# Kernel optimization log

Hardware: AMD Instinct MI355X
Metric: run time of the kernel (lower is better)

The kernel has to match this reference:

```python
import jax, jax.numpy as jnp
import numpy as np

B, S, D = 2, 2048, 1024
H, DH = 16, 64  # num_head, head_dim; H*DH == D


def setup_inputs() -> dict:
    key = jax.random.key(0)
    ks = jax.random.split(key, 10)
    stdv = 1.0 / np.sqrt(D)
    def lin(k):
        kw, kb = jax.random.split(k)
        W = jax.random.uniform(kw, (D, D), jnp.float32, -stdv, stdv)
        b = jax.random.uniform(kb, (D,), jnp.float32, -stdv, stdv)
        return W, b
    Wq, bq = lin(ks[0]); Wk, bk = lin(ks[1]); Wv, bv = lin(ks[2]); Wo, bo = lin(ks[3])
    x = jax.random.normal(ks[4], (B, S, D), jnp.float32)
    # causal mask: True = attend
    mask = jnp.tril(jnp.ones((S, S), jnp.bool_))
    mask = jnp.broadcast_to(mask, (B, S, S))
    return {"x": x, "mask": mask, "Wq": Wq, "bq": bq, "Wk": Wk, "bk": bk,
            "Wv": Wv, "bv": bv, "Wo": Wo, "bo": bo}


def _split_head(t):
    # [B,S,D] -> [B*H, S, DH]
    return t.reshape(B, S, H, DH).transpose(0, 2, 1, 3).reshape(B * H, S, DH)


def _concat_head(t):
    # [B*H, S, DH] -> [B, S, D]
    return t.reshape(B, H, S, DH).transpose(0, 2, 1, 3).reshape(B, S, D)


def reference(x, mask, Wq, bq, Wk, bk, Wv, bv, Wo, bo):
    q = _split_head(x @ Wq.T + bq)
    k = _split_head(x @ Wk.T + bk)
    v = _split_head(x @ Wv.T + bv)
    scale = 1.0 / jnp.sqrt(jnp.float32(DH))
    # scores: [B, H, S, S], masked softmax (flash-attention math, unfused ref)
    scores = jnp.einsum('nqd,nkd->nqk', q, k).reshape(B, H, S, S) * scale
    scores = jnp.where(mask[:, None, :, :], scores, jnp.finfo(scores.dtype).min)
    attn = jax.nn.softmax(scores, axis=-1)
    out = jnp.einsum('bhqk,nkd->bhqd', attn, v.reshape(B, H, S, DH).reshape(B * H, S, DH)).reshape(B * H, S, DH) if False else jnp.einsum('nqk,nkd->nqd', attn.reshape(B * H, S, S), v)
    return _concat_head(out) @ Wo.T + bo
```

## Files before the change

kernel.cpp:

```cpp
#include <hip/hip_runtime.h>
#include <cstdint>

#define S_LEN  2048
#define NH     16
#define DHEAD  64
#define DMODEL 1024

typedef __bf16 bf16x8 __attribute__((ext_vector_type(8)));
typedef __bf16 bf16x2 __attribute__((ext_vector_type(2)));
typedef float  f32x4  __attribute__((ext_vector_type(4)));

__device__ __forceinline__ unsigned short f2bf(float x) {
  union { float f; unsigned int u; } c; c.f = x;
  unsigned int u = c.u;
  return (unsigned short)((u + 0x7fffu + ((u >> 16) & 1u)) >> 16);
}

__device__ __forceinline__ unsigned int pkbf(float a, float b) {
#if __has_builtin(__builtin_amdgcn_cvt_pk_bf16_f32)
  bf16x2 r = __builtin_amdgcn_cvt_pk_bf16_f32(a, b);
  return *(unsigned int*)&r;
#else
  return (unsigned int)f2bf(a) | ((unsigned int)f2bf(b) << 16);
#endif
}

__device__ __forceinline__ unsigned short f2bf1(float x) {
#if __has_builtin(__builtin_amdgcn_cvt_pk_bf16_f32)
  bf16x2 r = __builtin_amdgcn_cvt_pk_bf16_f32(x, x);
  union { bf16x2 v; unsigned int u; } c; c.v = r;
  return (unsigned short)(c.u & 0xffffu);
#else
  return f2bf(x);
#endif
}

__device__ __forceinline__ __bf16 us2bf(unsigned short u) {
  union { unsigned short u; __bf16 b; } c; c.u = u; return c.b;
}

__device__ __forceinline__ void glds16(const void* g, void* l) {
  __builtin_amdgcn_global_load_lds(
      (const __attribute__((address_space(1))) void*)g,
      (__attribute__((address_space(3))) void*)l, 16, 0, 0);
}

__device__ __forceinline__ f32x4 mfma16(bf16x8 a, bf16x8 b, f32x4 c) {
  return __builtin_amdgcn_mfma_f32_16x16x32_bf16(a, b, c, 0, 0, 0);
}

__global__ void cvt_all(const float* __restrict__ x,
                        const float* __restrict__ Wq,
                        const float* __restrict__ Wk,
                        const float* __restrict__ Wv,
                        const float* __restrict__ Wo,
                        unsigned short* __restrict__ xb,
                        unsigned short* __restrict__ wqkv,
                        unsigned short* __restrict__ wo) {
  const int b = blockIdx.x;
  const float* src;
  unsigned short* dst;
  int off;
  if (b < 4096)      { src = x;  dst = xb;                off = b; }
  else if (b < 5120) { src = Wq; dst = wqkv;              off = b - 4096; }
  else if (b < 6144) { src = Wk; dst = wqkv + (1 << 20);  off = b - 5120; }
  else if (b < 7168) { src = Wv; dst = wqkv + (2 << 20);  off = b - 6144; }
  else               { src = Wo; dst = wo;                off = b - 7168; }
  const int i = (off * 256 + threadIdx.x) * 4;
  float4 v = *(const float4*)&src[i];
  uint2 r;
  r.x = pkbf(v.x, v.y);
  r.y = pkbf(v.z, v.w);
  *(uint2*)&dst[i] = r;
}

template<int MODE, int BN>
__global__ __launch_bounds__(256)
void gemm_bt(const unsigned short* __restrict__ A,
             const unsigned short* __restrict__ W,
             const float* __restrict__ bias0,
             const float* __restrict__ bias1,
             const float* __restrict__ bias2,
             unsigned short* __restrict__ Qt,
             unsigned short* __restrict__ Kb,
             unsigned short* __restrict__ Vt,
             float* __restrict__ Out,
             int K) {
  constexpr int JN = BN / 32;
  __shared__ __align__(16) unsigned short As[128 * 32];
  __shared__ __align__(16) unsigned short Bs[BN * 32];
  const int t    = threadIdx.x;
  const int lane = t & 63;
  const int w    = t >> 6;
  const int lr   = lane & 15, lq = lane >> 4;
  const int wm   = (w >> 1) * 64, wn = (w & 1) * (BN / 2);
  const int m0   = blockIdx.y * 128, n0 = blockIdx.x * BN;
  const int ra   = t >> 2, ca = (t & 3) * 8;

  f32x4 acc[4][JN] = {};

  const int kt = K >> 5;
  for (int kk = 0; kk < kt; ++kk) {
    const int k0 = kk << 5;
    glds16(A + (m0 + ra) * K + k0 + ca,      &As[ra * 32 + ca]);
    glds16(A + (m0 + 64 + ra) * K + k0 + ca, &As[(64 + ra) * 32 + ca]);
    glds16(W + (n0 + ra) * K + k0 + ca,      &Bs[ra * 32 + ca]);
    if (BN == 128)
      glds16(W + (n0 + 64 + ra) * K + k0 + ca, &Bs[(64 + ra) * 32 + ca]);
    __syncthreads();
    bf16x8 af[4], bg[JN];
#pragma unroll
    for (int i = 0; i < 4; ++i)
      af[i] = *(const bf16x8*)&As[(wm + i * 16 + lr) * 32 + lq * 8];
#pragma unroll
    for (int j = 0; j < JN; ++j)
      bg[j] = *(const bf16x8*)&Bs[(wn + j * 16 + lr) * 32 + lq * 8];
#pragma unroll
    for (int i = 0; i < 4; ++i)
#pragma unroll
      for (int j = 0; j < JN; ++j)
        acc[i][j] = mfma16(af[i], bg[j], acc[i][j]);
    __syncthreads();
  }

  if (MODE == 0) {
    const int tsel = n0 >> 10;
#pragma unroll
    for (int i = 0; i < 4; ++i) {
#pragma unroll
      for (int j = 0; j < JN; ++j) {
        const int mb = m0 + wm + i * 16 + lq * 4;
        const int n  = n0 + wn + j * 16 + lr;
        const int d  = n & 1023;
        const int bidx = mb >> 11, s = mb & (S_LEN - 1);
        const int h = d >> 6, dh = d & 63;
        const int bh = bidx * NH + h;
        const float bv0 = (tsel == 0) ? bias0[d] : ((tsel == 1) ? bias1[d] : bias2[d]);
        if (tsel == 0) {
          const float sc = 0.125f * 1.44269504088896f;
          uint2 pv;
          pv.x = pkbf((acc[i][j][0] + bv0) * sc, (acc[i][j][1] + bv0) * sc);
          pv.y = pkbf((acc[i][j][2] + bv0) * sc, (acc[i][j][3] + bv0) * sc);
          *(uint2*)&Qt[(bh * DHEAD + dh) * S_LEN + s] = pv;
        } else if (tsel == 2) {
          uint2 pv;
          pv.x = pkbf(acc[i][j][0] + bv0, acc[i][j][1] + bv0);
          pv.y = pkbf(acc[i][j][2] + bv0, acc[i][j][3] + bv0);
          *(uint2*)&Vt[(bh * DHEAD + dh) * S_LEN + s] = pv;
        } else {
#pragma unroll
          for (int r = 0; r < 4; ++r)
            Kb[(bh * S_LEN + s + r) * DHEAD + dh] = f2bf1(acc[i][j][r] + bv0);
        }
      }
    }
  } else {
#pragma unroll
    for (int i = 0; i < 4; ++i)
#pragma unroll
      for (int j = 0; j < JN; ++j)
#pragma unroll
        for (int r = 0; r < 4; ++r) {
          const int m = m0 + wm + i * 16 + lq * 4 + r;
          const int n = n0 + wn + j * 16 + lr;
          Out[m * DMODEL + n] = acc[i][j][r] + bias0[n];
        }
  }
}

__global__ __launch_bounds__(256, 4)
void flash_kernel(const unsigned short* __restrict__ Qt,
                  const unsigned short* __restrict__ Kb,
                  const unsigned short* __restrict__ Vt,
                  unsigned short* __restrict__ Ocat) {
  __shared__ __align__(16) unsigned short Ks[2][2][64 * 32];
  __shared__ __align__(16) unsigned short Vs[2][2][64 * 32];
  __shared__ __align__(16) unsigned short pls[4][1024];
  const int w = threadIdx.x >> 6, lane = threadIdx.x & 63;
  const int lr = lane & 15, lq = lane >> 4;
  const int bh = blockIdx.x;
  const int sb = 31 - blockIdx.y;
  const char* Kc = (const char*)(Kb + bh * (S_LEN * DHEAD));
  const char* Vc = (const char*)(Vt + bh * (DHEAD * S_LEN));
  const unsigned short* Qp = Qt + bh * (DHEAD * S_LEN);
  const int bb = bh >> 4, h = bh & 15;
  unsigned short* pw = &pls[w][0];
  const int swz = lr & 7;

  const int hh  = w & 1;
  const int rbb = (w >> 1) * 2;
  const int rlane = lane >> 2;
  const int clane = (lane & 3) * 16;

  const int q0 = sb * 64 + w * 16;
  bf16x8 qlo, qhi;
#pragma unroll
  for (int j = 0; j < 8; ++j) {
    qlo[j] = us2bf(Qp[(lq * 8 + j) * S_LEN + q0 + lr]);
    qhi[j] = us2bf(Qp[(32 + lq * 8 + j) * S_LEN + q0 + lr]);
  }

  bf16x8 ones;
#pragma unroll
  for (int j = 0; j < 8; ++j) ones[j] = (__bf16)1.0f;

  f32x4 o[4] = {};
  f32x4 lacc = {};
  const int nfull = sb;

  auto stage = [&](int buf, int sk0) {
#pragma unroll
    for (int j = 0; j < 2; ++j) {
      const int rb = rbb + j;
      glds16(Kc + (sk0 + rb * 16 + rlane) * 128 + hh * 64 + clane,
             &Ks[buf][hh][rb * 16 * 32]);
      glds16(Vc + (rb * 16 + rlane) * 4096 + (sk0 + hh * 32) * 2 + clane,
             &Vs[buf][hh][rb * 16 * 32]);
    }
  };

  stage(0, 0);
  for (int kt = 0; kt <= nfull; ++kt) {
    const int buf = kt & 1;
    __syncthreads();
    if (kt < nfull) stage(1 - buf, (kt + 1) << 6);

    f32x4 st[4] = {};
    const unsigned short* Kl = Ks[buf][0];
    const unsigned short* Kh = Ks[buf][1];
#pragma unroll
    for (int t = 0; t < 4; ++t) {
      st[t] = mfma16(*(const bf16x8*)&Kl[(t * 16 + lr) * 32 + lq * 8], qlo, st[t]);
      st[t] = mfma16(*(const bf16x8*)&Kh[(t * 16 + lr) * 32 + lq * 8], qhi, st[t]);
    }
    float p[4][4];
#pragma unroll
    for (int t = 0; t < 4; ++t)
#pragma unroll
      for (int r = 0; r < 4; ++r)
        p[t][r] = __builtin_amdgcn_exp2f(st[t][r]);
    if (kt == nfull) {
      const int q = q0 + lr, sk0 = kt << 6;
#pragma unroll
      for (int t = 0; t < 4; ++t)
#pragma unroll
        for (int r = 0; r < 4; ++r) {
          const int k = sk0 + t * 16 + lq * 4 + r;
          if (k > q) p[t][r] = 0.f;
        }
    }

#pragma unroll
    for (int t = 0; t < 4; ++t) {
      uint2 pk;
      pk.x = pkbf(p[t][0], p[t][1]);
      pk.y = pkbf(p[t][2], p[t][3]);
      const int g = t * 2 + (lq >> 1);
      *(uint2*)&pw[lr * 64 + ((g ^ swz) << 3) + ((lq & 1) << 2)] = pk;
    }
    const bf16x8 pf0 = *(const bf16x8*)&pw[lr * 64 + ((lq ^ swz) << 3)];
    const bf16x8 pf1 = *(const bf16x8*)&pw[lr * 64 + (((4 + lq) ^ swz) << 3)];
    const unsigned short* Vl = Vs[buf][0];
    const unsigned short* Vh = Vs[buf][1];
#pragma unroll
    for (int tt = 0; tt < 4; ++tt) {
      o[tt] = mfma16(*(const bf16x8*)&Vl[(tt * 16 + lr) * 32 + lq * 8], pf0, o[tt]);
      o[tt] = mfma16(*(const bf16x8*)&Vh[(tt * 16 + lr) * 32 + lq * 8], pf1, o[tt]);
    }
    lacc = mfma16(ones, pf0, lacc);
    lacc = mfma16(ones, pf1, lacc);
  }

  const float inv = 1.f / lacc[0];
#pragma unroll
  for (int tt = 0; tt < 4; ++tt) {
    uint2 ov;
    ov.x = pkbf(o[tt][0] * inv, o[tt][1] * inv);
    ov.y = pkbf(o[tt][2] * inv, o[tt][3] * inv);
    *(uint2*)&Ocat[(bb * S_LEN + q0 + lr) * DMODEL + h * DHEAD + tt * 16 + lq * 4] = ov;
  }
}

extern "C" void kernel_launch(void* const* d_in, const int* in_sizes, int n_in,
                              void* d_out, int out_size, void* d_ws, size_t ws_size,
                              hipStream_t stream) {
  const float* x  = (const float*)d_in[0];
  const float* Wq = (const float*)d_in[2];
  const float* bq = (const float*)d_in[3];
  const float* Wk = (const float*)d_in[4];
  const float* bk = (const float*)d_in[5];
  const float* Wv = (const float*)d_in[6];
  const float* bv = (const float*)d_in[7];
  const float* Wo = (const float*)d_in[8];
  const float* bo = (const float*)d_in[9];
  float* out = (float*)d_out;

  char* ws = (char*)d_ws;
  unsigned short* xb   = (unsigned short*)(ws);
  unsigned short* wqkv = (unsigned short*)(ws + (8ull  << 20));
  unsigned short* wo   = (unsigned short*)(ws + (14ull << 20));
  unsigned short* Qt   = (unsigned short*)(ws + (16ull << 20));
  unsigned short* Kb   = (unsigned short*)(ws + (24ull << 20));
  unsigned short* Vt   = (unsigned short*)(ws + (32ull << 20));
  unsigned short* Ocat = (unsigned short*)(ws + (40ull << 20));

  cvt_all<<<8192, 256, 0, stream>>>(x, Wq, Wk, Wv, Wo, xb, wqkv, wo);

  gemm_bt<0, 128><<<dim3(24, 32), 256, 0, stream>>>(xb, wqkv, bq, bk, bv,
                                                    Qt, Kb, Vt, nullptr, 1024);
  flash_kernel<<<dim3(32, 32), 256, 0, stream>>>(Qt, Kb, Vt, Ocat);
  gemm_bt<1, 64><<<dim3(16, 32), 256, 0, stream>>>(Ocat, wo, bo, nullptr, nullptr,
                                                   nullptr, nullptr, nullptr, out, 1024);
}
```

Before: 208.6 us.

## Split-K output projection with reduce kernel and swapped-operand K store

The output projection now uses a split-K GEMM with 128-wide tiles and two K halves, writing fp32 partials that a separate kernel sums and adds the bias to. This applies only when the workspace is large enough; otherwise the old path runs. The QKV GEMM also swaps the MFMA operands for K tiles so each lane holds four consecutive head-dim values and can write them with one 8-byte store instead of four scalar stores. In exchange, the split-K path adds an extra launch and 32MB of partial-sum traffic.

```diff
diff --git a/kernel.cpp b/kernel.cpp
--- a/kernel.cpp
+++ b/kernel.cpp
@@ -96,12 +96,15 @@
   const int wm   = (w >> 1) * 64, wn = (w & 1) * (BN / 2);
   const int m0   = blockIdx.y * 128, n0 = blockIdx.x * BN;
   const int ra   = t >> 2, ca = (t & 3) * 8;
+  const int kbase = (MODE == 2) ? (int)blockIdx.z * 512 : 0;
+  const int tsel = (MODE == 0) ? (n0 >> 10) : 0;
+  const bool swapped = (MODE == 0) && (tsel == 1);
 
   f32x4 acc[4][JN] = {};
 
-  const int kt = K >> 5;
-  for (int kk = 0; kk < kt; ++kk) {
-    const int k0 = kk << 5;
+  const int niter = (MODE == 2) ? 16 : (K >> 5);
+  for (int kk = 0; kk < niter; ++kk) {
+    const int k0 = kbase + (kk << 5);
     glds16(A + (m0 + ra) * K + k0 + ca,      &As[ra * 32 + ca]);
     glds16(A + (m0 + 64 + ra) * K + k0 + ca, &As[(64 + ra) * 32 + ca]);
     glds16(W + (n0 + ra) * K + k0 + ca,      &Bs[ra * 32 + ca]);
@@ -115,46 +118,68 @@
 #pragma unroll
     for (int j = 0; j < JN; ++j)
       bg[j] = *(const bf16x8*)&Bs[(wn + j * 16 + lr) * 32 + lq * 8];
-#pragma unroll
-    for (int i = 0; i < 4; ++i)
-#pragma unroll
-      for (int j = 0; j < JN; ++j)
-        acc[i][j] = mfma16(af[i], bg[j], acc[i][j]);
+    if (swapped) {
+#pragma unroll
+      for (int i = 0; i < 4; ++i)
+#pragma unroll
+        for (int j = 0; j < JN; ++j)
+          acc[i][j] = mfma16(bg[j], af[i], acc[i][j]);
+    } else {
+#pragma unroll
+      for (int i = 0; i < 4; ++i)
+#pragma unroll
+        for (int j = 0; j < JN; ++j)
+          acc[i][j] = mfma16(af[i], bg[j], acc[i][j]);
+    }
     __syncthreads();
   }
 
   if (MODE == 0) {
-    const int tsel = n0 >> 10;
-#pragma unroll
-    for (int i = 0; i < 4; ++i) {
-#pragma unroll
-      for (int j = 0; j < JN; ++j) {
-        const int mb = m0 + wm + i * 16 + lq * 4;
-        const int n  = n0 + wn + j * 16 + lr;
-        const int d  = n & 1023;
-        const int bidx = mb >> 11, s = mb & (S_LEN - 1);
-        const int h = d >> 6, dh = d & 63;
-        const int bh = bidx * NH + h;
-        const float bv0 = (tsel == 0) ? bias0[d] : ((tsel == 1) ? bias1[d] : bias2[d]);
-        if (tsel == 0) {
-          const float sc = 0.125f * 1.44269504088896f;
+    if (tsel == 1) {
+#pragma unroll
+      for (int i = 0; i < 4; ++i) {
+#pragma unroll
+        for (int j = 0; j < JN; ++j) {
+          const int m = m0 + wm + i * 16 + lr;
+          const int bidx = m >> 11, s = m & (S_LEN - 1);
+          const int dfull = (n0 & 1023) + wn + j * 16 + lq * 4;
+          const int h = dfull >> 6, dh = dfull & 63;
+          const int bh = bidx * NH + h;
+          const float4 bv4 = *(const float4*)&bias1[dfull];
           uint2 pv;
-          pv.x = pkbf((acc[i][j][0] + bv0) * sc, (acc[i][j][1] + bv0) * sc);
-          pv.y = pkbf((acc[i][j][2] + bv0) * sc, (acc[i][j][3] + bv0) * sc);
-          *(uint2*)&Qt[(bh * DHEAD + dh) * S_LEN + s] = pv;
-        } else if (tsel == 2) {
-          uint2 pv;
-          pv.x = pkbf(acc[i][j][0] + bv0, acc[i][j][1] + bv0);
-          pv.y = pkbf(acc[i][j][2] + bv0, acc[i][j][3] + bv0);
-          *(uint2*)&Vt[(bh * DHEAD + dh) * S_LEN + s] = pv;
-        } else {
-#pragma unroll
-          for (int r = 0; r < 4; ++r)
-            Kb[(bh * S_LEN + s + r) * DHEAD + dh] = f2bf1(acc[i][j][r] + bv0);
+          pv.x = pkbf(acc[i][j][0] + bv4.x, acc[i][j][1] + bv4.y);
+          pv.y = pkbf(acc[i][j][2] + bv4.z, acc[i][j][3] + bv4.w);
+          *(uint2*)&Kb[(bh * S_LEN + s) * DHEAD + dh] = pv;
         }
       }
-    }
-  } else {
+    } else {
+#pragma unroll
+      for (int i = 0; i < 4; ++i) {
+#pragma unroll
+        for (int j = 0; j < JN; ++j) {
+          const int mb = m0 + wm + i * 16 + lq * 4;
+          const int n  = n0 + wn + j * 16 + lr;
+          const int d  = n & 1023;
+          const int bidx = mb >> 11, s = mb & (S_LEN - 1);
+          const int h = d >> 6, dh = d & 63;
+          const int bh = bidx * NH + h;
+          const float bv0 = (tsel == 0) ? bias0[d] : bias2[d];
+          if (tsel == 0) {
+            const float sc = 0.125f * 1.44269504088896f;
+            uint2 pv;
+            pv.x = pkbf((acc[i][j][0] + bv0) * sc, (acc[i][j][1] + bv0) * sc);
+            pv.y = pkbf((acc[i][j][2] + bv0) * sc, (acc[i][j][3] + bv0) * sc);
+            *(uint2*)&Qt[(bh * DHEAD + dh) * S_LEN + s] = pv;
+          } else {
+            uint2 pv;
+            pv.x = pkbf(acc[i][j][0] + bv0, acc[i][j][1] + bv0);
+            pv.y = pkbf(acc[i][j][2] + bv0, acc[i][j][3] + bv0);
+            *(uint2*)&Vt[(bh * DHEAD + dh) * S_LEN + s] = pv;
+          }
+        }
+      }
+    }
+  } else if (MODE == 1) {
 #pragma unroll
     for (int i = 0; i < 4; ++i)
 #pragma unroll
@@ -165,7 +190,32 @@
           const int n = n0 + wn + j * 16 + lr;
           Out[m * DMODEL + n] = acc[i][j][r] + bias0[n];
         }
-  }
+  } else {
+    float* P = Out + (size_t)blockIdx.z * (4096 * 1024);
+#pragma unroll
+    for (int i = 0; i < 4; ++i)
+#pragma unroll
+      for (int j = 0; j < JN; ++j)
+#pragma unroll
+        for (int r = 0; r < 4; ++r) {
+          const int m = m0 + wm + i * 16 + lq * 4 + r;
+          const int n = n0 + wn + j * 16 + lr;
+          P[m * DMODEL + n] = acc[i][j][r];
+        }
+  }
+}
+
+__global__ void reduce_out(const float* __restrict__ part,
+                           const float* __restrict__ bias,
+                           float* __restrict__ out) {
+  const int i = (blockIdx.x * 256 + threadIdx.x) * 4;
+  float4 a = *(const float4*)&part[i];
+  float4 b = *(const float4*)&part[4096 * 1024 + i];
+  float4 c = *(const float4*)&bias[i & 1023];
+  float4 o;
+  o.x = a.x + b.x + c.x; o.y = a.y + b.y + c.y;
+  o.z = a.z + b.z + c.z; o.w = a.w + b.w + c.w;
+  *(float4*)&out[i] = o;
 }
 
 __global__ __launch_bounds__(256, 4)
@@ -303,12 +353,21 @@
   unsigned short* Kb   = (unsigned short*)(ws + (24ull << 20));
   unsigned short* Vt   = (unsigned short*)(ws + (32ull << 20));
   unsigned short* Ocat = (unsigned short*)(ws + (40ull << 20));
+  float*          part = (float*)(ws + (48ull << 20));
 
   cvt_all<<<8192, 256, 0, stream>>>(x, Wq, Wk, Wv, Wo, xb, wqkv, wo);
 
   gemm_bt<0, 128><<<dim3(24, 32), 256, 0, stream>>>(xb, wqkv, bq, bk, bv,
                                                     Qt, Kb, Vt, nullptr, 1024);
   flash_kernel<<<dim3(32, 32), 256, 0, stream>>>(Qt, Kb, Vt, Ocat);
-  gemm_bt<1, 64><<<dim3(16, 32), 256, 0, stream>>>(Ocat, wo, bo, nullptr, nullptr,
-                                                   nullptr, nullptr, nullptr, out, 1024);
-}
+
+  if (ws_size >= (80ull << 20)) {
+    gemm_bt<2, 128><<<dim3(8, 32, 2), 256, 0, stream>>>(Ocat, wo, nullptr, nullptr,
+                                                        nullptr, nullptr, nullptr,
+                                                        nullptr, part, 1024);
+    reduce_out<<<4096, 256, 0, stream>>>(part, bo, out);
+  } else {
+    gemm_bt<1, 64><<<dim3(16, 32), 256, 0, stream>>>(Ocat, wo, bo, nullptr, nullptr,
+                                                     nullptr, nullptr, nullptr, out, 1024);
+  }
+}
```

After: 239.6 us. 1.15x slower.
